# Kernel tuning notes

Measured on AMD Instinct MI355X. Metric: run time of the kernel, lower is better.

The kernel has to match this reference:

```python
import jax, jax.numpy as jnp
import numpy as np

N_NODES = 50000
DEG = 32
WIDTH = 128
DEPTH = 2
BATCH = 4096
EPS = 1e-12  # F.normalize default eps


def setup_inputs() -> dict:
    key = jax.random.key(0)
    k1, k2, k3, k4, k5, k6, k7 = jax.random.split(key, 7)
    nbd = jax.random.randint(k1, (N_NODES, DEG), 0, N_NODES, dtype=jnp.int32)
    node_idx = jax.random.randint(k2, (BATCH,), 0, N_NODES, dtype=jnp.int32)
    feats = jax.random.normal(k3, (BATCH, WIDTH), dtype=jnp.float32)
    s = 1.0 / np.sqrt(WIDTH)
    W_agg = jax.random.normal(k4, (WIDTH, WIDTH), dtype=jnp.float32) * s
    b_agg = jax.random.normal(k5, (WIDTH,), dtype=jnp.float32) * s
    W_lin = jax.random.normal(k6, (WIDTH, 2 * WIDTH), dtype=jnp.float32) * s
    b_lin = jax.random.normal(k7, (WIDTH,), dtype=jnp.float32) * s
    return {"nbd": nbd, "node_idx": node_idx, "feats": feats,
            "W_agg": W_agg, "b_agg": b_agg, "W_lin": W_lin, "b_lin": b_lin}


def reference(nbd, node_idx, feats, W_agg, b_agg, W_lin, b_lin):
    # H0: zero features for every graph node except the batch nodes (dict-of-zeros + row assignment in original)
    H = jnp.zeros((N_NODES, WIDTH), dtype=feats.dtype).at[node_idx].set(feats)
    for _ in range(DEPTH):  # combine Linear is weight-shared across hops (ModuleList([layer]*depth))
        # aggregator MLP applied once per node, then gathered per neighbor
        M = jax.nn.relu(H @ W_agg.T + b_agg)            # [N, d]
        agg = jnp.max(M[nbd], axis=1)                    # [N, deg, d] -> [N, d] max-pool aggregate
        h = jax.nn.relu(jnp.concatenate([H, agg], axis=-1) @ W_lin.T + b_lin)  # [N, d]
        norm = jnp.sqrt(jnp.sum(h * h, axis=-1, keepdims=True))
        H = h / jnp.maximum(norm, EPS)                   # F.normalize(dim=0) on 1d vector == per-row l2 norm
    return H[node_idx]                                   # [batch, width]
```

## Files before the change

kernel.cpp:

```cpp
#include <hip/hip_runtime.h>
#include <math.h>

#define N_NODES 50000
#define DEG 32
#define WIDTH 128
#define BATCH 4096
#define EPS 1e-12f

typedef __attribute__((ext_vector_type(8))) short short8;
typedef __attribute__((ext_vector_type(4))) float f32x4;
typedef unsigned short u16;

__device__ __forceinline__ u16 f2bf(float f) {
    unsigned x;
    __builtin_memcpy(&x, &f, 4);
    unsigned r = (x + 0x7fff + ((x >> 16) & 1)) >> 16;
    return (u16)r;
}
__device__ __forceinline__ unsigned pkmax_u16(unsigned a, unsigned b) {
    unsigned lo = (a & 0xffffu) > (b & 0xffffu) ? (a & 0xffffu) : (b & 0xffffu);
    unsigned hi = (a >> 16) > (b >> 16) ? (a >> 16) : (b >> 16);
    return lo | (hi << 16);
}
__device__ __forceinline__ short8 cvt8(const float* __restrict__ p) {
    float4 a0 = *(const float4*)p;
    float4 a1 = *(const float4*)(p + 4);
    short8 v;
    v[0] = (short)f2bf(a0.x); v[1] = (short)f2bf(a0.y);
    v[2] = (short)f2bf(a0.z); v[3] = (short)f2bf(a0.w);
    v[4] = (short)f2bf(a1.x); v[5] = (short)f2bf(a1.y);
    v[6] = (short)f2bf(a1.z); v[7] = (short)f2bf(a1.w);
    return v;
}

__global__ __launch_bounds__(512) void head_k(
    const float* __restrict__ feats, const float* __restrict__ W_agg,
    const float* __restrict__ W_lin, const float* __restrict__ b_agg,
    const int* __restrict__ node_idx, int* __restrict__ inv,
    u16* __restrict__ M0b, float* __restrict__ S) {
    __shared__ u16 wa[128 * 128];
    __shared__ u16 wl[128 * 128];

    int tid = threadIdx.x;
    int gid = blockIdx.x * 512 + tid;
    if (gid < BATCH) atomicMax(&inv[node_idx[gid]], gid);

#pragma unroll
    for (int it = 0; it < 4; ++it) {
        int c = tid + it * 512;
        int r = c >> 4, ch = c & 15;
        int sw = (ch * 16) ^ ((r & 7) << 4);
        *(short8*)((char*)wa + r * 256 + sw) = cvt8(W_agg + (size_t)r * 128 + ch * 8);
        *(short8*)((char*)wl + r * 256 + sw) = cvt8(W_lin + (size_t)r * 256 + ch * 8);
    }

    int w = tid >> 6, l = tid & 63, li = l & 15, kq = l >> 4;
    int r0 = blockIdx.x * 16;
    int arow = r0 + li;
    int col = w * 16 + li;

    short8 a[4];
#pragma unroll
    for (int kk = 0; kk < 4; ++kk)
        a[kk] = cvt8(feats + (size_t)arow * 128 + kk * 32 + kq * 8);
    __syncthreads();

    f32x4 am = (f32x4){0,0,0,0}, as = (f32x4){0,0,0,0};
#pragma unroll
    for (int kk = 0; kk < 4; ++kk) {
        int sw = (kk * 64 + kq * 16) ^ ((col & 7) << 4);
        short8 bm = *(const short8*)((char*)wa + col * 256 + sw);
        am = __builtin_amdgcn_mfma_f32_16x16x32_bf16(a[kk], bm, am, 0, 0, 0);
        short8 bs = *(const short8*)((char*)wl + col * 256 + sw);
        as = __builtin_amdgcn_mfma_f32_16x16x32_bf16(a[kk], bs, as, 0, 0, 0);
    }

    float ba = b_agg[col];
#pragma unroll
    for (int r = 0; r < 4; ++r) {
        int grow = r0 + kq * 4 + r;
        float t = am[r] + ba;
        t = t > 0.f ? t : 0.f;
        M0b[(size_t)grow * 128 + col] = f2bf(t);
        S[(size_t)grow * 128 + col] = as[r];
    }
}

__global__ __launch_bounds__(256) void agg1_k(
    const int* __restrict__ nbd, const int* __restrict__ inv,
    const u16* __restrict__ M0b, const float* __restrict__ b_agg,
    unsigned* __restrict__ AGG1u) {
    int wave = blockIdx.x * 4 + (threadIdx.x >> 6);
    int lane = threadIdx.x & 63;
    int n0 = wave * 2;

    int nb = nbd[(size_t)n0 * DEG + lane];
    int bi = inv[nb];
    unsigned long long warm = __ballot(bi >= 0);
    unsigned m0 = (unsigned)warm;
    unsigned m1 = (unsigned)(warm >> 32);

    float ba0 = b_agg[2 * lane], ba1 = b_agg[2 * lane + 1];
    ba0 = ba0 > 0.f ? ba0 : 0.f;
    ba1 = ba1 > 0.f ? ba1 : 0.f;
    unsigned rb = (unsigned)f2bf(ba0) | ((unsigned)f2bf(ba1) << 16);

    unsigned acc0 = (m0 != 0xffffffffu) ? rb : 0u;
    while (m0) {
        int pos = __builtin_ctz(m0);
        m0 &= m0 - 1;
        int bib = __shfl(bi, pos);
        acc0 = pkmax_u16(acc0, ((const unsigned*)(M0b + (size_t)bib * WIDTH))[lane]);
    }
    AGG1u[(size_t)n0 * 64 + lane] = acc0;

    unsigned acc1 = (m1 != 0xffffffffu) ? rb : 0u;
    while (m1) {
        int pos = __builtin_ctz(m1);
        m1 &= m1 - 1;
        int bib = __shfl(bi, 32 + pos);
        acc1 = pkmax_u16(acc1, ((const unsigned*)(M0b + (size_t)bib * WIDTH))[lane]);
    }
    AGG1u[(size_t)(n0 + 1) * 64 + lane] = acc1;
}

__global__ __launch_bounds__(512) void hop1mm_k(
    const u16* __restrict__ AGG1, const int* __restrict__ inv,
    const float* __restrict__ S, const float* __restrict__ b_lin,
    const float* __restrict__ b_agg,
    const float* __restrict__ W_lin, const float* __restrict__ W_agg,
    u16* __restrict__ H1g, u16* __restrict__ M1) {
    __shared__ u16 wlds[128 * 128];
    __shared__ u16 h1t[128 * 136];

    int tid = threadIdx.x;
    int w = tid >> 6, l = tid & 63, li = l & 15, kq = l >> 4;
    int row0 = blockIdx.x * 128;
    int lrow = w * 16 + li;
    int arow = row0 + lrow;
    if (arow > N_NODES - 1) arow = N_NODES - 1;

    short8 af[4];
#pragma unroll
    for (int kk = 0; kk < 4; ++kk)
        af[kk] = *(const short8*)(AGG1 + (size_t)arow * 128 + kk * 32 + kq * 8);

#pragma unroll
    for (int it = 0; it < 4; ++it) {
        int c = tid + it * 512;
        int r = c >> 4, ch = c & 15;
        *(short8*)((char*)wlds + r * 256 + ((ch * 16) ^ ((r & 7) << 4))) =
            cvt8(W_lin + (size_t)r * 256 + 128 + ch * 8);
    }
    __syncthreads();

    f32x4 h[8];
#pragma unroll
    for (int n = 0; n < 8; ++n) h[n] = (f32x4){0,0,0,0};
#pragma unroll
    for (int kk = 0; kk < 4; ++kk)
#pragma unroll
        for (int n = 0; n < 8; ++n) {
            int col = n * 16 + li;
            short8 b = *(const short8*)((char*)wlds + col * 256 +
                                        ((kk * 64 + kq * 16) ^ ((col & 7) << 4)));
            h[n] = __builtin_amdgcn_mfma_f32_16x16x32_bf16(af[kk], b, h[n], 0, 0, 0);
        }

    float blv[8];
#pragma unroll
    for (int n = 0; n < 8; ++n) blv[n] = b_lin[n * 16 + li];

#pragma unroll
    for (int r = 0; r < 4; ++r) {
        int lr = w * 16 + kq * 4 + r;
        int grow = row0 + lr;
        int growc = grow < N_NODES ? grow : N_NODES - 1;
        int bi = inv[growc];
        float v[8];
#pragma unroll
        for (int n = 0; n < 8; ++n) v[n] = h[n][r] + blv[n];
        if (bi >= 0) {
#pragma unroll
            for (int n = 0; n < 8; ++n) v[n] += S[(size_t)bi * 128 + n * 16 + li];
        }
        float p = 0.f;
#pragma unroll
        for (int n = 0; n < 8; ++n) {
            v[n] = fmaxf(v[n], 0.f);
            p += v[n] * v[n];
        }
        p += __shfl_xor(p, 1);
        p += __shfl_xor(p, 2);
        p += __shfl_xor(p, 4);
        p += __shfl_xor(p, 8);
        float sc = 1.0f / fmaxf(sqrtf(p), EPS);
        u16 vb[8];
#pragma unroll
        for (int n = 0; n < 8; ++n) vb[n] = f2bf(v[n] * sc);
        if (grow < N_NODES && bi >= 0) {
#pragma unroll
            for (int n = 0; n < 8; ++n) H1g[(size_t)grow * 128 + n * 16 + li] = vb[n];
        }
#pragma unroll
        for (int n = 0; n < 8; ++n) h1t[lr * 136 + n * 16 + li] = vb[n];
    }
    __syncthreads();

#pragma unroll
    for (int it = 0; it < 4; ++it) {
        int c = tid + it * 512;
        int r = c >> 4, ch = c & 15;
        *(short8*)((char*)wlds + r * 256 + ((ch * 16) ^ ((r & 7) << 4))) =
            cvt8(W_agg + (size_t)r * 128 + ch * 8);
    }
    __syncthreads();

    short8 af2[4];
#pragma unroll
    for (int kk = 0; kk < 4; ++kk)
        af2[kk] = *(const short8*)(h1t + lrow * 136 + kk * 32 + kq * 8);

    f32x4 m[8];
#pragma unroll
    for (int n = 0; n < 8; ++n) m[n] = (f32x4){0,0,0,0};
#pragma unroll
    for (int kk = 0; kk < 4; ++kk)
#pragma unroll
        for (int n = 0; n < 8; ++n) {
            int col = n * 16 + li;
            short8 b = *(const short8*)((char*)wlds + col * 256 +
                                        ((kk * 64 + kq * 16) ^ ((col & 7) << 4)));
            m[n] = __builtin_amdgcn_mfma_f32_16x16x32_bf16(af2[kk], b, m[n], 0, 0, 0);
        }

    float bav[8];
#pragma unroll
    for (int n = 0; n < 8; ++n) bav[n] = b_agg[n * 16 + li];
#pragma unroll
    for (int r = 0; r < 4; ++r) {
        int grow = row0 + w * 16 + kq * 4 + r;
        if (grow < N_NODES) {
#pragma unroll
            for (int n = 0; n < 8; ++n) {
                float t = m[n][r] + bav[n];
                t = t > 0.f ? t : 0.f;
                M1[(size_t)grow * 128 + n * 16 + li] = f2bf(t);
            }
        }
    }
}

__global__ __launch_bounds__(512) void tail_k(
    const int* __restrict__ nbd, const int* __restrict__ node_idx,
    const u16* __restrict__ H1g, const u16* __restrict__ M1,
    const float* __restrict__ W_lin, const float* __restrict__ b_lin,
    float* __restrict__ out) {
    __shared__ u16 wt[128 * 256];
    __shared__ u16 ab2[16 * 264];
    __shared__ float pn[128];
    __shared__ float pnt[16];

    int tid = threadIdx.x;
    int w = tid >> 6, l = tid & 63, li = l & 15, kq = l >> 4;
    int row0 = blockIdx.x * 16;

#pragma unroll
    for (int it = 0; it < 8; ++it) {
        int c = tid + it * 512;
        int r = c >> 5, ch = c & 31;
        *(short8*)((char*)wt + r * 512 + ((ch * 16) ^ ((r & 7) << 4))) =
            cvt8(W_lin + (size_t)r * 256 + ch * 8);
    }

#pragma unroll
    for (int rr = 0; rr < 2; ++rr) {
        int lr = w * 2 + rr;
        int i = row0 + lr;
        int n = node_idx[i];
        unsigned hv = ((const unsigned*)(H1g + (size_t)n * 128))[l];
        *(unsigned*)((char*)ab2 + lr * 528 + l * 4) = hv;
        int nb = (l < DEG) ? nbd[(size_t)n * DEG + l] : 0;
        unsigned acc = 0;
#pragma unroll
        for (int j = 0; j < DEG; ++j) {
            int bib = __shfl(nb, j);
            acc = pkmax_u16(acc, ((const unsigned*)(M1 + (size_t)bib * 128))[l]);
        }
        *(unsigned*)((char*)ab2 + lr * 528 + 256 + l * 4) = acc;
    }
    __syncthreads();

    int col = w * 16 + li;
    f32x4 acc4 = (f32x4){0,0,0,0};
#pragma unroll
    for (int kk = 0; kk < 8; ++kk) {
        short8 a = *(const short8*)((char*)ab2 + li * 528 + kk * 64 + kq * 16);
        short8 b = *(const short8*)((char*)wt + col * 512 +
                                    ((kk * 64 + kq * 16) ^ ((col & 7) << 4)));
        acc4 = __builtin_amdgcn_mfma_f32_16x16x32_bf16(a, b, acc4, 0, 0, 0);
    }

    float bl = b_lin[col];
    float v[4];
#pragma unroll
    for (int r = 0; r < 4; ++r) {
        v[r] = fmaxf(acc4[r] + bl, 0.f);
        float p = v[r] * v[r];
        p += __shfl_xor(p, 1);
        p += __shfl_xor(p, 2);
        p += __shfl_xor(p, 4);
        p += __shfl_xor(p, 8);
        if (li == 0) pn[w * 16 + kq * 4 + r] = p;
    }
    __syncthreads();
    if (tid < 16) {
        float s = 0.f;
#pragma unroll
        for (int ww = 0; ww < 8; ++ww) s += pn[ww * 16 + tid];
        pnt[tid] = s;
    }
    __syncthreads();
#pragma unroll
    for (int r = 0; r < 4; ++r) {
        int row = kq * 4 + r;
        float sc = 1.0f / fmaxf(sqrtf(pnt[row]), EPS);
        out[(size_t)(row0 + row) * 128 + col] = v[r] * sc;
    }
}

extern "C" void kernel_launch(void* const* d_in, const int* in_sizes, int n_in,
                              void* d_out, int out_size, void* d_ws, size_t ws_size,
                              hipStream_t stream) {
    const int*   nbd      = (const int*)d_in[0];
    const int*   node_idx = (const int*)d_in[1];
    const float* feats    = (const float*)d_in[2];
    const float* W_agg    = (const float*)d_in[3];
    const float* b_agg    = (const float*)d_in[4];
    const float* W_lin    = (const float*)d_in[5];
    const float* b_lin    = (const float*)d_in[6];
    float* out = (float*)d_out;

    char* base = (char*)d_ws;
    size_t off = 0;
    int* inv  = (int*)(base + off);  off += 50048 * 4;
    u16* M0b  = (u16*)(base + off);  off += (size_t)BATCH * 128 * 2;
    float* S  = (float*)(base + off); off += (size_t)BATCH * 128 * 4;
    u16* AGG1 = (u16*)(base + off);  off += (size_t)N_NODES * 128 * 2;
    u16* H1g  = (u16*)(base + off);  off += (size_t)N_NODES * 128 * 2;
    u16* M1   = (u16*)(base + off);  off += (size_t)N_NODES * 128 * 2;

    hipMemsetAsync(inv, 0xFF, 50048 * 4, stream);

    head_k<<<BATCH / 16, 512, 0, stream>>>(feats, W_agg, W_lin, b_agg, node_idx, inv, M0b, S);

    agg1_k<<<N_NODES / 8, 256, 0, stream>>>(nbd, inv, M0b, b_agg, (unsigned*)AGG1);

    hop1mm_k<<<(N_NODES + 127) / 128, 512, 0, stream>>>(
        AGG1, inv, S, b_lin, b_agg, W_lin, W_agg, H1g, M1);

    tail_k<<<BATCH / 16, 512, 0, stream>>>(nbd, node_idx, H1g, M1, W_lin, b_lin, out);
}
```

Measured before the change: 55.38 us.

## Split fused hop-1 kernel into two kernels with 64-row tiles

Splits the fused hop-1 kernel (combine linear + normalize, then aggregator MLP) into two kernels: one writes normalized H1 for all nodes to global memory, the other reads it back and computes M1. Tiles shrink to 64 rows with two waves splitting the output columns, and the row norm is combined across waves through shared memory. This doubles the grid and lowers per-wave accumulator registers to raise occupancy. The cost is an extra launch, an extra global round-trip of the full H1 array, and repeated weight conversion into shared memory per block.

```diff
diff --git a/kernel.cpp b/kernel.cpp
--- a/kernel.cpp
+++ b/kernel.cpp
@@ -124,19 +124,18 @@
     AGG1u[(size_t)(n0 + 1) * 64 + lane] = acc1;
 }
 
-__global__ __launch_bounds__(512) void hop1mm_k(
+__global__ __launch_bounds__(512) void hop1a_k(
     const u16* __restrict__ AGG1, const int* __restrict__ inv,
     const float* __restrict__ S, const float* __restrict__ b_lin,
-    const float* __restrict__ b_agg,
-    const float* __restrict__ W_lin, const float* __restrict__ W_agg,
-    u16* __restrict__ H1g, u16* __restrict__ M1) {
+    const float* __restrict__ W_lin, u16* __restrict__ H1g) {
     __shared__ u16 wlds[128 * 128];
-    __shared__ u16 h1t[128 * 136];
+    __shared__ float pnorm[2 * 64];
 
     int tid = threadIdx.x;
     int w = tid >> 6, l = tid & 63, li = l & 15, kq = l >> 4;
-    int row0 = blockIdx.x * 128;
-    int lrow = w * 16 + li;
+    int rg = w >> 1, cg = w & 1;
+    int row0 = blockIdx.x * 64;
+    int lrow = rg * 16 + li;
     int arow = row0 + lrow;
     if (arow > N_NODES - 1) arow = N_NODES - 1;
 
@@ -154,58 +153,81 @@
     }
     __syncthreads();
 
-    f32x4 h[8];
-#pragma unroll
-    for (int n = 0; n < 8; ++n) h[n] = (f32x4){0,0,0,0};
-#pragma unroll
-    for (int kk = 0; kk < 4; ++kk)
-#pragma unroll
-        for (int n = 0; n < 8; ++n) {
-            int col = n * 16 + li;
+    f32x4 h[4];
+#pragma unroll
+    for (int n = 0; n < 4; ++n) h[n] = (f32x4){0,0,0,0};
+#pragma unroll
+    for (int kk = 0; kk < 4; ++kk)
+#pragma unroll
+        for (int n = 0; n < 4; ++n) {
+            int col = cg * 64 + n * 16 + li;
             short8 b = *(const short8*)((char*)wlds + col * 256 +
                                         ((kk * 64 + kq * 16) ^ ((col & 7) << 4)));
             h[n] = __builtin_amdgcn_mfma_f32_16x16x32_bf16(af[kk], b, h[n], 0, 0, 0);
         }
 
-    float blv[8];
-#pragma unroll
-    for (int n = 0; n < 8; ++n) blv[n] = b_lin[n * 16 + li];
-
-#pragma unroll
-    for (int r = 0; r < 4; ++r) {
-        int lr = w * 16 + kq * 4 + r;
+    float blv[4];
+#pragma unroll
+    for (int n = 0; n < 4; ++n) blv[n] = b_lin[cg * 64 + n * 16 + li];
+
+    float v[4][4];
+#pragma unroll
+    for (int r = 0; r < 4; ++r) {
+        int lr = rg * 16 + kq * 4 + r;
         int grow = row0 + lr;
         int growc = grow < N_NODES ? grow : N_NODES - 1;
         int bi = inv[growc];
-        float v[8];
-#pragma unroll
-        for (int n = 0; n < 8; ++n) v[n] = h[n][r] + blv[n];
+#pragma unroll
+        for (int n = 0; n < 4; ++n) v[r][n] = h[n][r] + blv[n];
         if (bi >= 0) {
 #pragma unroll
-            for (int n = 0; n < 8; ++n) v[n] += S[(size_t)bi * 128 + n * 16 + li];
+            for (int n = 0; n < 4; ++n)
+                v[r][n] += S[(size_t)bi * 128 + cg * 64 + n * 16 + li];
         }
         float p = 0.f;
 #pragma unroll
-        for (int n = 0; n < 8; ++n) {
-            v[n] = fmaxf(v[n], 0.f);
-            p += v[n] * v[n];
+        for (int n = 0; n < 4; ++n) {
+            v[r][n] = fmaxf(v[r][n], 0.f);
+            p += v[r][n] * v[r][n];
         }
         p += __shfl_xor(p, 1);
         p += __shfl_xor(p, 2);
         p += __shfl_xor(p, 4);
         p += __shfl_xor(p, 8);
+        if (li == 0) pnorm[cg * 64 + lr] = p;
+    }
+    __syncthreads();
+
+#pragma unroll
+    for (int r = 0; r < 4; ++r) {
+        int lr = rg * 16 + kq * 4 + r;
+        int grow = row0 + lr;
+        float p = pnorm[lr] + pnorm[64 + lr];
         float sc = 1.0f / fmaxf(sqrtf(p), EPS);
-        u16 vb[8];
-#pragma unroll
-        for (int n = 0; n < 8; ++n) vb[n] = f2bf(v[n] * sc);
-        if (grow < N_NODES && bi >= 0) {
-#pragma unroll
-            for (int n = 0; n < 8; ++n) H1g[(size_t)grow * 128 + n * 16 + li] = vb[n];
-        }
-#pragma unroll
-        for (int n = 0; n < 8; ++n) h1t[lr * 136 + n * 16 + li] = vb[n];
-    }
-    __syncthreads();
+        if (grow < N_NODES) {
+#pragma unroll
+            for (int n = 0; n < 4; ++n)
+                H1g[(size_t)grow * 128 + cg * 64 + n * 16 + li] = f2bf(v[r][n] * sc);
+        }
+    }
+}
+
+__global__ __launch_bounds__(512) void m1_k(
+    const u16* __restrict__ H1g, const float* __restrict__ b_agg,
+    const float* __restrict__ W_agg, u16* __restrict__ M1) {
+    __shared__ u16 wlds[128 * 128];
+
+    int tid = threadIdx.x;
+    int w = tid >> 6, l = tid & 63, li = l & 15, kq = l >> 4;
+    int rg = w >> 1, cg = w & 1;
+    int row0 = blockIdx.x * 64;
+    int arow = row0 + rg * 16 + li;
+    if (arow > N_NODES - 1) arow = N_NODES - 1;
+
+    short8 af[4];
+#pragma unroll
+    for (int kk = 0; kk < 4; ++kk)
+        af[kk] = *(const short8*)(H1g + (size_t)arow * 128 + kk * 32 + kq * 8);
 
 #pragma unroll
     for (int it = 0; it < 4; ++it) {
@@ -216,36 +238,31 @@
     }
     __syncthreads();
 
-    short8 af2[4];
-#pragma unroll
-    for (int kk = 0; kk < 4; ++kk)
-        af2[kk] = *(const short8*)(h1t + lrow * 136 + kk * 32 + kq * 8);
-
-    f32x4 m[8];
-#pragma unroll
-    for (int n = 0; n < 8; ++n) m[n] = (f32x4){0,0,0,0};
-#pragma unroll
-    for (int kk = 0; kk < 4; ++kk)
-#pragma unroll
-        for (int n = 0; n < 8; ++n) {
-            int col = n * 16 + li;
+    f32x4 m[4];
+#pragma unroll
+    for (int n = 0; n < 4; ++n) m[n] = (f32x4){0,0,0,0};
+#pragma unroll
+    for (int kk = 0; kk < 4; ++kk)
+#pragma unroll
+        for (int n = 0; n < 4; ++n) {
+            int col = cg * 64 + n * 16 + li;
             short8 b = *(const short8*)((char*)wlds + col * 256 +
                                         ((kk * 64 + kq * 16) ^ ((col & 7) << 4)));
-            m[n] = __builtin_amdgcn_mfma_f32_16x16x32_bf16(af2[kk], b, m[n], 0, 0, 0);
-        }
-
-    float bav[8];
-#pragma unroll
-    for (int n = 0; n < 8; ++n) bav[n] = b_agg[n * 16 + li];
-#pragma unroll
-    for (int r = 0; r < 4; ++r) {
-        int grow = row0 + w * 16 + kq * 4 + r;
+            m[n] = __builtin_amdgcn_mfma_f32_16x16x32_bf16(af[kk], b, m[n], 0, 0, 0);
+        }
+
+    float bav[4];
+#pragma unroll
+    for (int n = 0; n < 4; ++n) bav[n] = b_agg[cg * 64 + n * 16 + li];
+#pragma unroll
+    for (int r = 0; r < 4; ++r) {
+        int grow = row0 + rg * 16 + kq * 4 + r;
         if (grow < N_NODES) {
 #pragma unroll
-            for (int n = 0; n < 8; ++n) {
+            for (int n = 0; n < 4; ++n) {
                 float t = m[n][r] + bav[n];
                 t = t > 0.f ? t : 0.f;
-                M1[(size_t)grow * 128 + n * 16 + li] = f2bf(t);
+                M1[(size_t)grow * 128 + cg * 64 + n * 16 + li] = f2bf(t);
             }
         }
     }
@@ -343,12 +360,12 @@
 
     char* base = (char*)d_ws;
     size_t off = 0;
-    int* inv  = (int*)(base + off);  off += 50048 * 4;
-    u16* M0b  = (u16*)(base + off);  off += (size_t)BATCH * 128 * 2;
+    int* inv  = (int*)(base + off);   off += 50048 * 4;
+    u16* M0b  = (u16*)(base + off);   off += (size_t)BATCH * 128 * 2;
     float* S  = (float*)(base + off); off += (size_t)BATCH * 128 * 4;
-    u16* AGG1 = (u16*)(base + off);  off += (size_t)N_NODES * 128 * 2;
-    u16* H1g  = (u16*)(base + off);  off += (size_t)N_NODES * 128 * 2;
-    u16* M1   = (u16*)(base + off);  off += (size_t)N_NODES * 128 * 2;
+    u16* AGG1 = (u16*)(base + off);   off += (size_t)N_NODES * 128 * 2;
+    u16* H1g  = (u16*)(base + off);   off += (size_t)N_NODES * 128 * 2;
+    u16* M1   = (u16*)(base + off);   off += (size_t)N_NODES * 128 * 2;
 
     hipMemsetAsync(inv, 0xFF, 50048 * 4, stream);
 
@@ -356,8 +373,9 @@
 
     agg1_k<<<N_NODES / 8, 256, 0, stream>>>(nbd, inv, M0b, b_agg, (unsigned*)AGG1);
 
-    hop1mm_k<<<(N_NODES + 127) / 128, 512, 0, stream>>>(
-        AGG1, inv, S, b_lin, b_agg, W_lin, W_agg, H1g, M1);
+    hop1a_k<<<(N_NODES + 63) / 64, 512, 0, stream>>>(AGG1, inv, S, b_lin, W_lin, H1g);
+
+    m1_k<<<(N_NODES + 63) / 64, 512, 0, stream>>>(H1g, b_agg, W_agg, M1);
 
     tail_k<<<BATCH / 16, 512, 0, stream>>>(nbd, node_idx, H1g, M1, W_lin, b_lin, out);
 }
```

New measurement: 63.47 us. +14.6%, slower.

## Fuse four stage kernels into one cooperative kernel with grid syncs

Applied to the files above, without the earlier changes.

Replaces the four separate launches (head, aggregation, hop-1 matmul, tail) with one persistent cooperative kernel of 256 blocks that separates the stages with grid.sync(). The aggregation and hop-1 stages become grid-stride loops over nodes and tiles. The tail stage's LDS weight buffer is halved by loading the two halves of W_lin one after the other. The aim is to remove per-launch overhead and inter-kernel gaps, at the cost of grid-wide barriers and a fixed grid of 256 blocks that may under-occupy the large stages. If the cooperative launch fails, the code falls back to the original four launches.

```diff
diff --git a/kernel.cpp b/kernel.cpp
--- a/kernel.cpp
+++ b/kernel.cpp
@@ -1,11 +1,15 @@
 #include <hip/hip_runtime.h>
+#include <hip/hip_cooperative_groups.h>
 #include <math.h>
+
+namespace cg = cooperative_groups;
 
 #define N_NODES 50000
 #define DEG 32
 #define WIDTH 128
 #define BATCH 4096
 #define EPS 1e-12f
+#define NBLK 256
 
 typedef __attribute__((ext_vector_type(8))) short short8;
 typedef __attribute__((ext_vector_type(4))) float f32x4;
@@ -40,11 +44,9 @@
     u16* __restrict__ M0b, float* __restrict__ S) {
     __shared__ u16 wa[128 * 128];
     __shared__ u16 wl[128 * 128];
-
     int tid = threadIdx.x;
     int gid = blockIdx.x * 512 + tid;
     if (gid < BATCH) atomicMax(&inv[node_idx[gid]], gid);
-
 #pragma unroll
     for (int it = 0; it < 4; ++it) {
         int c = tid + it * 512;
@@ -53,18 +55,15 @@
         *(short8*)((char*)wa + r * 256 + sw) = cvt8(W_agg + (size_t)r * 128 + ch * 8);
         *(short8*)((char*)wl + r * 256 + sw) = cvt8(W_lin + (size_t)r * 256 + ch * 8);
     }
-
     int w = tid >> 6, l = tid & 63, li = l & 15, kq = l >> 4;
     int r0 = blockIdx.x * 16;
     int arow = r0 + li;
     int col = w * 16 + li;
-
     short8 a[4];
 #pragma unroll
     for (int kk = 0; kk < 4; ++kk)
         a[kk] = cvt8(feats + (size_t)arow * 128 + kk * 32 + kq * 8);
     __syncthreads();
-
     f32x4 am = (f32x4){0,0,0,0}, as = (f32x4){0,0,0,0};
 #pragma unroll
     for (int kk = 0; kk < 4; ++kk) {
@@ -74,7 +73,6 @@
         short8 bs = *(const short8*)((char*)wl + col * 256 + sw);
         as = __builtin_amdgcn_mfma_f32_16x16x32_bf16(a[kk], bs, as, 0, 0, 0);
     }
-
     float ba = b_agg[col];
 #pragma unroll
     for (int r = 0; r < 4; ++r) {
@@ -93,18 +91,15 @@
     int wave = blockIdx.x * 4 + (threadIdx.x >> 6);
     int lane = threadIdx.x & 63;
     int n0 = wave * 2;
-
     int nb = nbd[(size_t)n0 * DEG + lane];
     int bi = inv[nb];
     unsigned long long warm = __ballot(bi >= 0);
     unsigned m0 = (unsigned)warm;
     unsigned m1 = (unsigned)(warm >> 32);
-
     float ba0 = b_agg[2 * lane], ba1 = b_agg[2 * lane + 1];
     ba0 = ba0 > 0.f ? ba0 : 0.f;
     ba1 = ba1 > 0.f ? ba1 : 0.f;
     unsigned rb = (unsigned)f2bf(ba0) | ((unsigned)f2bf(ba1) << 16);
-
     unsigned acc0 = (m0 != 0xffffffffu) ? rb : 0u;
     while (m0) {
         int pos = __builtin_ctz(m0);
@@ -113,7 +108,6 @@
         acc0 = pkmax_u16(acc0, ((const unsigned*)(M0b + (size_t)bib * WIDTH))[lane]);
     }
     AGG1u[(size_t)n0 * 64 + lane] = acc0;
-
     unsigned acc1 = (m1 != 0xffffffffu) ? rb : 0u;
     while (m1) {
         int pos = __builtin_ctz(m1);
@@ -132,19 +126,16 @@
     u16* __restrict__ H1g, u16* __restrict__ M1) {
     __shared__ u16 wlds[128 * 128];
     __shared__ u16 h1t[128 * 136];
-
     int tid = threadIdx.x;
     int w = tid >> 6, l = tid & 63, li = l & 15, kq = l >> 4;
     int row0 = blockIdx.x * 128;
     int lrow = w * 16 + li;
     int arow = row0 + lrow;
     if (arow > N_NODES - 1) arow = N_NODES - 1;
-
     short8 af[4];
 #pragma unroll
     for (int kk = 0; kk < 4; ++kk)
         af[kk] = *(const short8*)(AGG1 + (size_t)arow * 128 + kk * 32 + kq * 8);
-
 #pragma unroll
     for (int it = 0; it < 4; ++it) {
         int c = tid + it * 512;
@@ -153,7 +144,6 @@
             cvt8(W_lin + (size_t)r * 256 + 128 + ch * 8);
     }
     __syncthreads();
-
     f32x4 h[8];
 #pragma unroll
     for (int n = 0; n < 8; ++n) h[n] = (f32x4){0,0,0,0};
@@ -166,11 +156,9 @@
                                         ((kk * 64 + kq * 16) ^ ((col & 7) << 4)));
             h[n] = __builtin_amdgcn_mfma_f32_16x16x32_bf16(af[kk], b, h[n], 0, 0, 0);
         }
-
     float blv[8];
 #pragma unroll
     for (int n = 0; n < 8; ++n) blv[n] = b_lin[n * 16 + li];
-
 #pragma unroll
     for (int r = 0; r < 4; ++r) {
         int lr = w * 16 + kq * 4 + r;
@@ -206,7 +194,6 @@
         for (int n = 0; n < 8; ++n) h1t[lr * 136 + n * 16 + li] = vb[n];
     }
     __syncthreads();
-
 #pragma unroll
     for (int it = 0; it < 4; ++it) {
         int c = tid + it * 512;
@@ -215,12 +202,10 @@
             cvt8(W_agg + (size_t)r * 128 + ch * 8);
     }
     __syncthreads();
-
     short8 af2[4];
 #pragma unroll
     for (int kk = 0; kk < 4; ++kk)
         af2[kk] = *(const short8*)(h1t + lrow * 136 + kk * 32 + kq * 8);
-
     f32x4 m[8];
 #pragma unroll
     for (int n = 0; n < 8; ++n) m[n] = (f32x4){0,0,0,0};
@@ -233,7 +218,6 @@
                                         ((kk * 64 + kq * 16) ^ ((col & 7) << 4)));
             m[n] = __builtin_amdgcn_mfma_f32_16x16x32_bf16(af2[kk], b, m[n], 0, 0, 0);
         }
-
     float bav[8];
 #pragma unroll
     for (int n = 0; n < 8; ++n) bav[n] = b_agg[n * 16 + li];
@@ -260,11 +244,9 @@
     __shared__ u16 ab2[16 * 264];
     __shared__ float pn[128];
     __shared__ float pnt[16];
-
     int tid = threadIdx.x;
     int w = tid >> 6, l = tid & 63, li = l & 15, kq = l >> 4;
     int row0 = blockIdx.x * 16;
-
 #pragma unroll
     for (int it = 0; it < 8; ++it) {
         int c = tid + it * 512;
@@ -272,7 +254,6 @@
         *(short8*)((char*)wt + r * 512 + ((ch * 16) ^ ((r & 7) << 4))) =
             cvt8(W_lin + (size_t)r * 256 + ch * 8);
     }
-
 #pragma unroll
     for (int rr = 0; rr < 2; ++rr) {
         int lr = w * 2 + rr;
@@ -290,7 +271,6 @@
         *(unsigned*)((char*)ab2 + lr * 528 + 256 + l * 4) = acc;
     }
     __syncthreads();
-
     int col = w * 16 + li;
     f32x4 acc4 = (f32x4){0,0,0,0};
 #pragma unroll
@@ -300,7 +280,6 @@
                                     ((kk * 64 + kq * 16) ^ ((col & 7) << 4)));
         acc4 = __builtin_amdgcn_mfma_f32_16x16x32_bf16(a, b, acc4, 0, 0, 0);
     }
-
     float bl = b_lin[col];
     float v[4];
 #pragma unroll
@@ -326,6 +305,294 @@
         int row = kq * 4 + r;
         float sc = 1.0f / fmaxf(sqrtf(pnt[row]), EPS);
         out[(size_t)(row0 + row) * 128 + col] = v[r] * sc;
+    }
+}
+
+__global__ __launch_bounds__(512) void fused_k(
+    const int* __restrict__ nbd, const int* __restrict__ node_idx,
+    const float* __restrict__ feats, const float* __restrict__ W_agg,
+    const float* __restrict__ b_agg, const float* __restrict__ W_lin,
+    const float* __restrict__ b_lin, int* __restrict__ inv,
+    u16* __restrict__ M0b, float* __restrict__ S, unsigned* __restrict__ AGG1u,
+    u16* __restrict__ H1g, u16* __restrict__ M1, float* __restrict__ out) {
+    __shared__ __align__(16) char lds[67584];
+    cg::grid_group grid = cg::this_grid();
+
+    const int tid = threadIdx.x;
+    const int bid = blockIdx.x;
+    const int w = tid >> 6, l = tid & 63, li = l & 15, kq = l >> 4;
+
+    {
+        int gid = bid * 512 + tid;
+        if (gid < BATCH) atomicMax(&inv[node_idx[gid]], gid);
+    }
+    {
+        u16* wa = (u16*)lds;
+        u16* wl = (u16*)(lds + 32768);
+#pragma unroll
+        for (int it = 0; it < 4; ++it) {
+            int c = tid + it * 512;
+            int r = c >> 4, ch = c & 15;
+            int sw = (ch * 16) ^ ((r & 7) << 4);
+            *(short8*)((char*)wa + r * 256 + sw) = cvt8(W_agg + (size_t)r * 128 + ch * 8);
+            *(short8*)((char*)wl + r * 256 + sw) = cvt8(W_lin + (size_t)r * 256 + ch * 8);
+        }
+        int r0 = bid * 16;
+        int arow = r0 + li;
+        int col = w * 16 + li;
+        short8 a[4];
+#pragma unroll
+        for (int kk = 0; kk < 4; ++kk)
+            a[kk] = cvt8(feats + (size_t)arow * 128 + kk * 32 + kq * 8);
+        __syncthreads();
+        f32x4 am = (f32x4){0,0,0,0}, as = (f32x4){0,0,0,0};
+#pragma unroll
+        for (int kk = 0; kk < 4; ++kk) {
+            int sw = (kk * 64 + kq * 16) ^ ((col & 7) << 4);
+            short8 bm = *(const short8*)((char*)wa + col * 256 + sw);
+            am = __builtin_amdgcn_mfma_f32_16x16x32_bf16(a[kk], bm, am, 0, 0, 0);
+            short8 bs = *(const short8*)((char*)wl + col * 256 + sw);
+            as = __builtin_amdgcn_mfma_f32_16x16x32_bf16(a[kk], bs, as, 0, 0, 0);
+        }
+        float ba = b_agg[col];
+#pragma unroll
+        for (int r = 0; r < 4; ++r) {
+            int grow = r0 + kq * 4 + r;
+            float t = am[r] + ba;
+            t = t > 0.f ? t : 0.f;
+            M0b[(size_t)grow * 128 + col] = f2bf(t);
+            S[(size_t)grow * 128 + col] = as[r];
+        }
+    }
+    grid.sync();
+
+    {
+        int nw = gridDim.x * 8;
+        int wgid = bid * 8 + w;
+        float ba0 = b_agg[2 * l], ba1 = b_agg[2 * l + 1];
+        ba0 = ba0 > 0.f ? ba0 : 0.f;
+        ba1 = ba1 > 0.f ? ba1 : 0.f;
+        unsigned rb = (unsigned)f2bf(ba0) | ((unsigned)f2bf(ba1) << 16);
+        for (int p = wgid; p < N_NODES / 2; p += nw) {
+            int n0 = p * 2;
+            int nb = nbd[(size_t)n0 * DEG + l];
+            int bi = inv[nb];
+            unsigned long long warm = __ballot(bi >= 0);
+            unsigned m0 = (unsigned)warm;
+            unsigned m1m = (unsigned)(warm >> 32);
+            unsigned acc0 = (m0 != 0xffffffffu) ? rb : 0u;
+            while (m0) {
+                int pos = __builtin_ctz(m0);
+                m0 &= m0 - 1;
+                int bib = __shfl(bi, pos);
+                acc0 = pkmax_u16(acc0, ((const unsigned*)(M0b + (size_t)bib * WIDTH))[l]);
+            }
+            AGG1u[(size_t)n0 * 64 + l] = acc0;
+            unsigned acc1 = (m1m != 0xffffffffu) ? rb : 0u;
+            while (m1m) {
+                int pos = __builtin_ctz(m1m);
+                m1m &= m1m - 1;
+                int bib = __shfl(bi, 32 + pos);
+                acc1 = pkmax_u16(acc1, ((const unsigned*)(M0b + (size_t)bib * WIDTH))[l]);
+            }
+            AGG1u[(size_t)(n0 + 1) * 64 + l] = acc1;
+        }
+    }
+    grid.sync();
+
+    for (int t = bid; t < (N_NODES + 127) / 128; t += NBLK) {
+        __syncthreads();
+        u16* wlds = (u16*)lds;
+        u16* h1t = (u16*)(lds + 32768);
+        int row0 = t * 128;
+        int lrow = w * 16 + li;
+        int arow = row0 + lrow;
+        if (arow > N_NODES - 1) arow = N_NODES - 1;
+        short8 af[4];
+#pragma unroll
+        for (int kk = 0; kk < 4; ++kk)
+            af[kk] = *(const short8*)((const u16*)AGG1u + (size_t)arow * 128 + kk * 32 + kq * 8);
+#pragma unroll
+        for (int it = 0; it < 4; ++it) {
+            int c = tid + it * 512;
+            int r = c >> 4, ch = c & 15;
+            *(short8*)((char*)wlds + r * 256 + ((ch * 16) ^ ((r & 7) << 4))) =
+                cvt8(W_lin + (size_t)r * 256 + 128 + ch * 8);
+        }
+        __syncthreads();
+        f32x4 h[8];
+#pragma unroll
+        for (int n = 0; n < 8; ++n) h[n] = (f32x4){0,0,0,0};
+#pragma unroll
+        for (int kk = 0; kk < 4; ++kk)
+#pragma unroll
+            for (int n = 0; n < 8; ++n) {
+                int col = n * 16 + li;
+                short8 b = *(const short8*)((char*)wlds + col * 256 +
+                                            ((kk * 64 + kq * 16) ^ ((col & 7) << 4)));
+                h[n] = __builtin_amdgcn_mfma_f32_16x16x32_bf16(af[kk], b, h[n], 0, 0, 0);
+            }
+        float blv[8];
+#pragma unroll
+        for (int n = 0; n < 8; ++n) blv[n] = b_lin[n * 16 + li];
+#pragma unroll
+        for (int r = 0; r < 4; ++r) {
+            int lr = w * 16 + kq * 4 + r;
+            int grow = row0 + lr;
+            int growc = grow < N_NODES ? grow : N_NODES - 1;
+            int bi = inv[growc];
+            float v[8];
+#pragma unroll
+            for (int n = 0; n < 8; ++n) v[n] = h[n][r] + blv[n];
+            if (bi >= 0) {
+#pragma unroll
+                for (int n = 0; n < 8; ++n) v[n] += S[(size_t)bi * 128 + n * 16 + li];
+            }
+            float p = 0.f;
+#pragma unroll
+            for (int n = 0; n < 8; ++n) {
+                v[n] = fmaxf(v[n], 0.f);
+                p += v[n] * v[n];
+            }
+            p += __shfl_xor(p, 1);
+            p += __shfl_xor(p, 2);
+            p += __shfl_xor(p, 4);
+            p += __shfl_xor(p, 8);
+            float sc = 1.0f / fmaxf(sqrtf(p), EPS);
+            u16 vb[8];
+#pragma unroll
+            for (int n = 0; n < 8; ++n) vb[n] = f2bf(v[n] * sc);
+            if (grow < N_NODES && bi >= 0) {
+#pragma unroll
+                for (int n = 0; n < 8; ++n) H1g[(size_t)grow * 128 + n * 16 + li] = vb[n];
+            }
+#pragma unroll
+            for (int n = 0; n < 8; ++n) h1t[lr * 136 + n * 16 + li] = vb[n];
+        }
+        __syncthreads();
+#pragma unroll
+        for (int it = 0; it < 4; ++it) {
+            int c = tid + it * 512;
+            int r = c >> 4, ch = c & 15;
+            *(short8*)((char*)wlds + r * 256 + ((ch * 16) ^ ((r & 7) << 4))) =
+                cvt8(W_agg + (size_t)r * 128 + ch * 8);
+        }
+        __syncthreads();
+        short8 af2[4];
+#pragma unroll
+        for (int kk = 0; kk < 4; ++kk)
+            af2[kk] = *(const short8*)(h1t + lrow * 136 + kk * 32 + kq * 8);
+        f32x4 m[8];
+#pragma unroll
+        for (int n = 0; n < 8; ++n) m[n] = (f32x4){0,0,0,0};
+#pragma unroll
+        for (int kk = 0; kk < 4; ++kk)
+#pragma unroll
+            for (int n = 0; n < 8; ++n) {
+                int col = n * 16 + li;
+                short8 b = *(const short8*)((char*)wlds + col * 256 +
+                                            ((kk * 64 + kq * 16) ^ ((col & 7) << 4)));
+                m[n] = __builtin_amdgcn_mfma_f32_16x16x32_bf16(af2[kk], b, m[n], 0, 0, 0);
+            }
+        float bav[8];
+#pragma unroll
+        for (int n = 0; n < 8; ++n) bav[n] = b_agg[n * 16 + li];
+#pragma unroll
+        for (int r = 0; r < 4; ++r) {
+            int grow = row0 + w * 16 + kq * 4 + r;
+            if (grow < N_NODES) {
+#pragma unroll
+                for (int n = 0; n < 8; ++n) {
+                    float t2 = m[n][r] + bav[n];
+                    t2 = t2 > 0.f ? t2 : 0.f;
+                    M1[(size_t)grow * 128 + n * 16 + li] = f2bf(t2);
+                }
+            }
+        }
+    }
+    grid.sync();
+
+    {
+        u16* wt = (u16*)lds;
+        u16* ab2 = (u16*)(lds + 32768);
+        float* pn = (float*)(lds + 32768 + 8448);
+        float* pnt = (float*)(lds + 32768 + 8448 + 512);
+        int row0 = bid * 16;
+#pragma unroll
+        for (int it = 0; it < 4; ++it) {
+            int c = tid + it * 512;
+            int r = c >> 4, ch = c & 15;
+            *(short8*)((char*)wt + r * 256 + ((ch * 16) ^ ((r & 7) << 4))) =
+                cvt8(W_lin + (size_t)r * 256 + ch * 8);
+        }
+#pragma unroll
+        for (int rr = 0; rr < 2; ++rr) {
+            int lr = w * 2 + rr;
+            int i = row0 + lr;
+            int n = node_idx[i];
+            unsigned hv = ((const unsigned*)(H1g + (size_t)n * 128))[l];
+            *(unsigned*)((char*)ab2 + lr * 528 + l * 4) = hv;
+            int nb = (l < DEG) ? nbd[(size_t)n * DEG + l] : 0;
+            unsigned acc = 0;
+#pragma unroll
+            for (int j = 0; j < DEG; ++j) {
+                int bib = __shfl(nb, j);
+                acc = pkmax_u16(acc, ((const unsigned*)(M1 + (size_t)bib * 128))[l]);
+            }
+            *(unsigned*)((char*)ab2 + lr * 528 + 256 + l * 4) = acc;
+        }
+        __syncthreads();
+        int col = w * 16 + li;
+        f32x4 acc4 = (f32x4){0,0,0,0};
+#pragma unroll
+        for (int kk = 0; kk < 4; ++kk) {
+            short8 a = *(const short8*)((char*)ab2 + li * 528 + kk * 64 + kq * 16);
+            short8 b = *(const short8*)((char*)wt + col * 256 +
+                                        ((kk * 64 + kq * 16) ^ ((col & 7) << 4)));
+            acc4 = __builtin_amdgcn_mfma_f32_16x16x32_bf16(a, b, acc4, 0, 0, 0);
+        }
+        __syncthreads();
+#pragma unroll
+        for (int it = 0; it < 4; ++it) {
+            int c = tid + it * 512;
+            int r = c >> 4, ch = c & 15;
+            *(short8*)((char*)wt + r * 256 + ((ch * 16) ^ ((r & 7) << 4))) =
+                cvt8(W_lin + (size_t)r * 256 + 128 + ch * 8);
+        }
+        __syncthreads();
+#pragma unroll
+        for (int kk = 0; kk < 4; ++kk) {
+            short8 a = *(const short8*)((char*)ab2 + li * 528 + 256 + kk * 64 + kq * 16);
+            short8 b = *(const short8*)((char*)wt + col * 256 +
+                                        ((kk * 64 + kq * 16) ^ ((col & 7) << 4)));
+            acc4 = __builtin_amdgcn_mfma_f32_16x16x32_bf16(a, b, acc4, 0, 0, 0);
+        }
+        float bl = b_lin[col];
+        float v[4];
+#pragma unroll
+        for (int r = 0; r < 4; ++r) {
+            v[r] = fmaxf(acc4[r] + bl, 0.f);
+            float p = v[r] * v[r];
+            p += __shfl_xor(p, 1);
+            p += __shfl_xor(p, 2);
+            p += __shfl_xor(p, 4);
+            p += __shfl_xor(p, 8);
+            if (li == 0) pn[w * 16 + kq * 4 + r] = p;
+        }
+        __syncthreads();
+        if (tid < 16) {
+            float s = 0.f;
+#pragma unroll
+            for (int ww = 0; ww < 8; ++ww) s += pn[ww * 16 + tid];
+            pnt[tid] = s;
+        }
+        __syncthreads();
+#pragma unroll
+        for (int r = 0; r < 4; ++r) {
+            int row = kq * 4 + r;
+            float sc = 1.0f / fmaxf(sqrtf(pnt[row]), EPS);
+            out[(size_t)(row0 + row) * 128 + col] = v[r] * sc;
+        }
     }
 }
 
@@ -343,21 +610,28 @@
 
     char* base = (char*)d_ws;
     size_t off = 0;
-    int* inv  = (int*)(base + off);  off += 50048 * 4;
-    u16* M0b  = (u16*)(base + off);  off += (size_t)BATCH * 128 * 2;
-    float* S  = (float*)(base + off); off += (size_t)BATCH * 128 * 4;
-    u16* AGG1 = (u16*)(base + off);  off += (size_t)N_NODES * 128 * 2;
-    u16* H1g  = (u16*)(base + off);  off += (size_t)N_NODES * 128 * 2;
-    u16* M1   = (u16*)(base + off);  off += (size_t)N_NODES * 128 * 2;
+    int* inv       = (int*)(base + off);      off += 50048 * 4;
+    u16* M0b       = (u16*)(base + off);      off += (size_t)BATCH * 128 * 2;
+    float* S       = (float*)(base + off);    off += (size_t)BATCH * 128 * 4;
+    unsigned* AGG1 = (unsigned*)(base + off); off += (size_t)N_NODES * 128 * 2;
+    u16* H1g       = (u16*)(base + off);      off += (size_t)N_NODES * 128 * 2;
+    u16* M1        = (u16*)(base + off);      off += (size_t)N_NODES * 128 * 2;
 
     hipMemsetAsync(inv, 0xFF, 50048 * 4, stream);
 
-    head_k<<<BATCH / 16, 512, 0, stream>>>(feats, W_agg, W_lin, b_agg, node_idx, inv, M0b, S);
-
-    agg1_k<<<N_NODES / 8, 256, 0, stream>>>(nbd, inv, M0b, b_agg, (unsigned*)AGG1);
-
-    hop1mm_k<<<(N_NODES + 127) / 128, 512, 0, stream>>>(
-        AGG1, inv, S, b_lin, b_agg, W_lin, W_agg, H1g, M1);
-
-    tail_k<<<BATCH / 16, 512, 0, stream>>>(nbd, node_idx, H1g, M1, W_lin, b_lin, out);
-}
+    void* args[] = {
+        (void*)&nbd, (void*)&node_idx, (void*)&feats, (void*)&W_agg, (void*)&b_agg,
+        (void*)&W_lin, (void*)&b_lin, (void*)&inv, (void*)&M0b, (void*)&S,
+        (void*)&AGG1, (void*)&H1g, (void*)&M1, (void*)&out
+    };
+    hipError_t err = hipLaunchCooperativeKernel((const void*)fused_k, dim3(NBLK),
+                                                dim3(512), args, 0, stream);
+    if (err != hipSuccess) {
+        head_k<<<BATCH / 16, 512, 0, stream>>>(feats, W_agg, W_lin, b_agg,
+                                               node_idx, inv, M0b, S);
+        agg1_k<<<N_NODES / 8, 256, 0, stream>>>(nbd, inv, (const u16*)M0b, b_agg, AGG1);
+        hop1mm_k<<<(N_NODES + 127) / 128, 512, 0, stream>>>(
+            (const u16*)AGG1, inv, S, b_lin, b_agg, W_lin, W_agg, H1g, M1);
+        tail_k<<<BATCH / 16, 512, 0, stream>>>(nbd, node_idx, H1g, M1, W_lin, b_lin, out);
+    }
+}
```

After: 165.3 us. 199% more time.
